# Performance work log

Hardware: AMD Instinct MI355X
Metric: run time of the kernel (lower is better)

## Reference

```python
import jax, jax.numpy as jnp
import numpy as np


def setup_inputs() -> dict:
    key = jax.random.key(0)
    X = jax.random.normal(key, (8, 4096, 64), dtype=jnp.float32)
    return {"X": X}


def reference(X) -> jnp.ndarray:
    # raw_weights: [B, S, S] = X @ X^T
    raw_weights = jnp.einsum("bsd,btd->bst", X, X)
    # softmax over last (key) dim, as in F.softmax(raw_weights, dim=2)
    weights = jax.nn.softmax(raw_weights, axis=2)
    # y: [B, S, D]
    y = jnp.einsum("bst,btd->bsd", weights, X).astype(jnp.float32)
    return y
```

## Files before the change

### kernel.cpp

```cpp
#include <hip/hip_runtime.h>
#include <hip/hip_bf16.h>
#include <stdint.h>


#define BB 8
#define SS 4096
#define DD 64
#define KVB 64
#define LDK 72

typedef __attribute__((ext_vector_type(8))) _Float16 f16x8;
typedef __attribute__((ext_vector_type(8))) __bf16 bf16x8;
typedef __attribute__((ext_vector_type(4))) float f32x4;

__device__ __forceinline__ _Float16 f2h(float f) { return (_Float16)f; }
__device__ __forceinline__ __bf16 f2bf(float f) { return (__bf16)f; }
__device__ __forceinline__ float exp2g(float x) { return __builtin_amdgcn_exp2f(x); }

__device__ __forceinline__ void gload_lds16(const _Float16* g, _Float16* l) {
  __builtin_amdgcn_global_load_lds(
      (const __attribute__((address_space(1))) uint32_t*)g,
      (__attribute__((address_space(3))) uint32_t*)l, 16, 0, 0);
}

__global__ __launch_bounds__(256)
void prepack(const float* __restrict__ X, _Float16* __restrict__ Gh,
             _Float16* __restrict__ Gl, _Float16* __restrict__ Gt) {
  const int b  = blockIdx.x >> 6;
  const int s0 = (blockIdx.x & 63) * 64;
  const int t  = threadIdx.x;
  const int r  = t >> 2;
  const int cq = t & 3;

  __shared__ float Xs[64][68];

  {
    const float* src = X + ((size_t)b * SS + s0 + r) * DD + cq * 16;
    float4 f0 = ((const float4*)src)[0];
    float4 f1 = ((const float4*)src)[1];
    float4 f2 = ((const float4*)src)[2];
    float4 f3 = ((const float4*)src)[3];
    *(float4*)&Xs[r][cq * 16 + 0]  = f0;
    *(float4*)&Xs[r][cq * 16 + 4]  = f1;
    *(float4*)&Xs[r][cq * 16 + 8]  = f2;
    *(float4*)&Xs[r][cq * 16 + 12] = f3;
  }
  __syncthreads();

  const size_t rowbase = ((size_t)b * SS + s0 + r) * DD;
#pragma unroll
  for (int cc = 0; cc < 2; ++cc) {
    const int c = cq * 2 + cc;
    f16x8 h, lo;
#pragma unroll
    for (int j = 0; j < 8; ++j) {
      float v = Xs[r][c * 8 + j];
      _Float16 hv = f2h(v);
      h[j]  = hv;
      lo[j] = f2h(v - (float)hv);
    }
    const int csw = c ^ (r & 7);
    *(f16x8*)(Gh + rowbase + csw * 8) = h;
    *(f16x8*)(Gl + rowbase + csw * 8) = lo;
  }

  const size_t tbase = ((size_t)b * DD + r) * SS + s0;
#pragma unroll
  for (int cc = 0; cc < 2; ++cc) {
    const int c  = cq * 2 + cc;
    const int g  = c >> 2;
    const int qt = c & 3;
    f16x8 h;
#pragma unroll
    for (int j = 0; j < 8; ++j) {
      const int kvl = 32 * g + 16 * (j >> 2) + 4 * qt + (j & 3);
      h[j] = f2h(Xs[kvl][r]);
    }
    const int csw = c ^ (r & 7);
    *(f16x8*)(Gt + tbase + csw * 8) = h;
  }
}

template <int NSPLIT>
__global__ __launch_bounds__(256, 4)
void attn_fwd5(float* __restrict__ Y, const _Float16* __restrict__ Gh,
               const _Float16* __restrict__ Gl, const _Float16* __restrict__ Gt,
               float* __restrict__ Opart, float* __restrict__ ML) {
  const int b    = blockIdx.x & 7;
  const int q0   = ((blockIdx.x >> 3) & 63) * 64;
  const int half = (NSPLIT == 2) ? (blockIdx.x >> 9) : 0;
  const int kvbase = half * (SS / NSPLIT);
  const int NT2    = (SS / NSPLIT) / KVB;

  const int tid  = threadIdx.x;
  const int wid  = tid >> 6;
  const int lane = tid & 63;
  const int lrow = lane & 15;
  const int qt   = lane >> 4;
  const int key  = lane & 7;

  __shared__ __align__(16) _Float16 Kh[2][KVB][DD];
  __shared__ __align__(16) _Float16 Vt[2][DD][KVB];

  const _Float16* GhB = Gh + (size_t)b * SS * DD;
  const _Float16* GlB = Gl + (size_t)b * SS * DD;
  const _Float16* GtB = Gt + (size_t)b * DD * SS;

  const float LOG2E = 1.4426950408889634f;
  f16x8 qh[2], ql[2];
  {
    const int s = q0 + wid * 16 + lrow;
    const _Float16* rh = GhB + (size_t)s * DD;
    const _Float16* rl = GlB + (size_t)s * DD;
#pragma unroll
    for (int kd = 0; kd < 2; ++kd) {
      const int ch = ((kd * 4 + qt) ^ key) * 8;
      f16x8 h  = *(const f16x8*)(rh + ch);
      f16x8 lo = *(const f16x8*)(rl + ch);
#pragma unroll
      for (int j = 0; j < 8; ++j) {
        float q = ((float)h[j] + (float)lo[j]) * LOG2E;
        _Float16 hv = f2h(q);
        qh[kd][j] = hv;
        ql[kd][j] = f2h(q - (float)hv);
      }
    }
  }

  float m = -INFINITY, lsum = 0.f;
  f32x4 accO[4];
#pragma unroll
  for (int dt = 0; dt < 4; ++dt)
#pragma unroll
    for (int r = 0; r < 4; ++r) accO[dt][r] = 0.f;

  const int lr8 = lane >> 3;
  const int co  = (lane & 7) * 8;

  auto stage = [&](int t, int bufi) {
    const int kv0 = kvbase + t * KVB;
#pragma unroll
    for (int i = 0; i < 2; ++i) {
      const int r0 = wid * 16 + i * 8;
      const int gr = kv0 + r0 + lr8;
      gload_lds16(GhB + (size_t)gr * DD + co, &Kh[bufi][r0][0]);
      gload_lds16(GtB + (size_t)(r0 + lr8) * SS + kv0 + co, &Vt[bufi][r0][0]);
    }
  };

  stage(0, 0);
  __syncthreads();

  for (int t = 0; t < NT2; ++t) {
    const int buf = t & 1;
    if (t + 1 < NT2) stage(t + 1, buf ^ 1);

    f32x4 S[4];
#pragma unroll
    for (int s = 0; s < 4; ++s)
#pragma unroll
      for (int r = 0; r < 4; ++r) S[s][r] = 0.f;

    __builtin_amdgcn_s_setprio(1);
#pragma unroll
    for (int kd = 0; kd < 2; ++kd) {
      const int ch = ((kd * 4 + qt) ^ key) * 8;
#pragma unroll
      for (int s = 0; s < 4; ++s) {
        const int row = s * 16 + lrow;
        f16x8 ah = *(const f16x8*)&Kh[buf][row][ch];
        S[s] = __builtin_amdgcn_mfma_f32_16x16x32_f16(ah, qh[kd], S[s], 0, 0, 0);
        S[s] = __builtin_amdgcn_mfma_f32_16x16x32_f16(ah, ql[kd], S[s], 0, 0, 0);
      }
    }
    __builtin_amdgcn_s_setprio(0);

    float v0 = fmaxf(fmaxf(S[0][0], S[0][1]), fmaxf(S[0][2], S[0][3]));
    float v1 = fmaxf(fmaxf(S[1][0], S[1][1]), fmaxf(S[1][2], S[1][3]));
    float v2 = fmaxf(fmaxf(S[2][0], S[2][1]), fmaxf(S[2][2], S[2][3]));
    float v3 = fmaxf(fmaxf(S[3][0], S[3][1]), fmaxf(S[3][2], S[3][3]));
    float vm = fmaxf(fmaxf(v0, v1), fmaxf(v2, v3));
    vm = fmaxf(vm, __shfl_xor(vm, 16));
    vm = fmaxf(vm, __shfl_xor(vm, 32));
    const float mnew = fmaxf(m, vm);
    const float sc   = exp2g(m - mnew);
    m = mnew;

    float rs = 0.f;
#pragma unroll
    for (int s = 0; s < 4; ++s) {
      f32x4 p;
#pragma unroll
      for (int r = 0; r < 4; ++r) p[r] = exp2g(S[s][r] - mnew);
      S[s] = p;
      rs += (p[0] + p[1]) + (p[2] + p[3]);
    }
    rs += __shfl_xor(rs, 16);
    rs += __shfl_xor(rs, 32);
    lsum = lsum * sc + rs;
#pragma unroll
    for (int dt = 0; dt < 4; ++dt)
#pragma unroll
      for (int r = 0; r < 4; ++r) accO[dt][r] *= sc;

    f16x8 pb0, pb1;
#pragma unroll
    for (int j = 0; j < 4; ++j) {
      pb0[j]     = f2h(S[0][j]);
      pb0[j + 4] = f2h(S[1][j]);
      pb1[j]     = f2h(S[2][j]);
      pb1[j + 4] = f2h(S[3][j]);
    }

    __builtin_amdgcn_s_setprio(1);
#pragma unroll
    for (int dt = 0; dt < 4; ++dt) {
      const _Float16* vr = &Vt[buf][dt * 16 + lrow][0];
#pragma unroll
      for (int g = 0; g < 2; ++g) {
        f16x8 av = *(const f16x8*)(vr + ((4 * g + qt) ^ key) * 8);
        accO[dt] = __builtin_amdgcn_mfma_f32_16x16x32_f16(
            av, g ? pb1 : pb0, accO[dt], 0, 0, 0);
      }
    }
    __builtin_amdgcn_s_setprio(0);

    __syncthreads();
  }

  const int srow = q0 + wid * 16 + lrow;
  if (NSPLIT == 1) {
    const float inv = 1.f / lsum;
    float* Yr = Y + ((size_t)b * SS + srow) * DD;
#pragma unroll
    for (int dt = 0; dt < 4; ++dt)
#pragma unroll
      for (int r = 0; r < 4; ++r)
        Yr[dt * 16 + qt * 4 + r] = accO[dt][r] * inv;
  } else {
    float* Or = Opart + (((size_t)half * BB + b) * SS + srow) * DD;
#pragma unroll
    for (int dt = 0; dt < 4; ++dt)
#pragma unroll
      for (int r = 0; r < 4; ++r)
        Or[dt * 16 + qt * 4 + r] = accO[dt][r];
    if (qt == 0) {
      float* mlr = ML + (((size_t)half * BB + b) * SS + srow) * 2;
      mlr[0] = m;
      mlr[1] = lsum;
    }
  }
}

__global__ __launch_bounds__(256)
void combine2(float* __restrict__ Y, const float* __restrict__ Opart,
              const float* __restrict__ ML) {
  const size_t NROW = (size_t)BB * SS;
  const int tid = threadIdx.x;
  const size_t row = (size_t)blockIdx.x * 32 + (tid >> 3);
  const int d0 = (tid & 7) * 8;

  const float m0 = ML[row * 2 + 0];
  const float l0 = ML[row * 2 + 1];
  const float m1 = ML[(NROW + row) * 2 + 0];
  const float l1 = ML[(NROW + row) * 2 + 1];
  const float M  = fmaxf(m0, m1);
  const float w0 = exp2g(m0 - M);
  const float w1 = exp2g(m1 - M);
  const float inv = 1.f / (w0 * l0 + w1 * l1);

  const float* o0 = Opart + row * DD + d0;
  const float* o1 = Opart + (NROW + row) * DD + d0;
  float* y = Y + row * DD + d0;
#pragma unroll
  for (int h = 0; h < 2; ++h) {
    float4 a = ((const float4*)o0)[h];
    float4 c = ((const float4*)o1)[h];
    float4 o;
    o.x = (w0 * a.x + w1 * c.x) * inv;
    o.y = (w0 * a.y + w1 * c.y) * inv;
    o.z = (w0 * a.z + w1 * c.z) * inv;
    o.w = (w0 * a.w + w1 * c.w) * inv;
    ((float4*)y)[h] = o;
  }
}

__global__ __launch_bounds__(256, 2)
void attn_fwd_r2(const float* __restrict__ X, float* __restrict__ Y) {
  const int nqb = SS / 64;
  const int b  = blockIdx.x / nqb;
  const int q0 = (blockIdx.x % nqb) * 64;
  const int tid  = threadIdx.x;
  const int wid  = tid >> 6;
  const int lane = tid & 63;
  const int lrow = lane & 15;
  const int lhi  = lane >> 4;

  __shared__ __align__(16) __bf16 Xh[KVB][LDK];
  __shared__ __align__(16) __bf16 Xl[KVB][LDK];
  __shared__ __align__(16) __bf16 XT[DD][LDK];
  __shared__ __align__(16) __bf16 Pl[4][16][LDK];

  const float* Xb = X + (size_t)b * SS * DD;

  bf16x8 qh[2], ql[2];
  {
    const float* qp = Xb + (size_t)(q0 + wid * 16 + lrow) * DD;
#pragma unroll
    for (int kk = 0; kk < 2; ++kk) {
      const float4* p = reinterpret_cast<const float4*>(qp + kk * 32 + lhi * 8);
      float4 f0 = p[0], f1 = p[1];
      float v[8] = {f0.x, f0.y, f0.z, f0.w, f1.x, f1.y, f1.z, f1.w};
      bf16x8 h, lo;
#pragma unroll
      for (int j = 0; j < 8; ++j) {
        __bf16 hv = f2bf(v[j]);
        h[j]  = hv;
        lo[j] = f2bf(v[j] - (float)hv);
      }
      qh[kk] = h;
      ql[kk] = lo;
    }
  }

  float m[4], lsum[4];
  f32x4 accO[4];
#pragma unroll
  for (int r = 0; r < 4; ++r) { m[r] = -INFINITY; lsum[r] = 0.f; }
#pragma unroll
  for (int c = 0; c < 4; ++c)
#pragma unroll
    for (int r = 0; r < 4; ++r) accO[c][r] = 0.f;

  for (int kv0 = 0; kv0 < SS; kv0 += KVB) {
    __syncthreads();
    {
      const int r  = tid >> 2;
      const int c0 = (tid & 3) * 16;
      const float* src = Xb + (size_t)(kv0 + r) * DD + c0;
#pragma unroll
      for (int half = 0; half < 2; ++half) {
        const float4* p = reinterpret_cast<const float4*>(src + half * 8);
        float4 f0 = p[0], f1 = p[1];
        float v[8] = {f0.x, f0.y, f0.z, f0.w, f1.x, f1.y, f1.z, f1.w};
        bf16x8 h, lo;
#pragma unroll
        for (int j = 0; j < 8; ++j) {
          __bf16 hv = f2bf(v[j]);
          h[j]  = hv;
          lo[j] = f2bf(v[j] - (float)hv);
        }
        *reinterpret_cast<bf16x8*>(&Xh[r][c0 + half * 8]) = h;
        *reinterpret_cast<bf16x8*>(&Xl[r][c0 + half * 8]) = lo;
#pragma unroll
        for (int j = 0; j < 8; ++j) XT[c0 + half * 8 + j][r] = h[j];
      }
    }
    __syncthreads();

    f32x4 Sacc[4];
#pragma unroll
    for (int c = 0; c < 4; ++c)
#pragma unroll
      for (int r = 0; r < 4; ++r) Sacc[c][r] = 0.f;

#pragma unroll
    for (int kk = 0; kk < 2; ++kk) {
#pragma unroll
      for (int c = 0; c < 4; ++c) {
        bf16x8 bh = *reinterpret_cast<bf16x8*>(&Xh[c * 16 + lrow][kk * 32 + lhi * 8]);
        bf16x8 bl = *reinterpret_cast<bf16x8*>(&Xl[c * 16 + lrow][kk * 32 + lhi * 8]);
        Sacc[c] = __builtin_amdgcn_mfma_f32_16x16x32_bf16(qh[kk], bh, Sacc[c], 0, 0, 0);
        Sacc[c] = __builtin_amdgcn_mfma_f32_16x16x32_bf16(qh[kk], bl, Sacc[c], 0, 0, 0);
        Sacc[c] = __builtin_amdgcn_mfma_f32_16x16x32_bf16(ql[kk], bh, Sacc[c], 0, 0, 0);
      }
    }

#pragma unroll
    for (int r = 0; r < 4; ++r) {
      float v = fmaxf(fmaxf(Sacc[0][r], Sacc[1][r]), fmaxf(Sacc[2][r], Sacc[3][r]));
#pragma unroll
      for (int off = 1; off < 16; off <<= 1)
        v = fmaxf(v, __shfl_xor(v, off, 16));
      const float mnew  = fmaxf(m[r], v);
      const float scale = __expf(m[r] - mnew);
      m[r] = mnew;

      float rowsum = 0.f;
#pragma unroll
      for (int c = 0; c < 4; ++c) {
        float p = __expf(Sacc[c][r] - mnew);
        rowsum += p;
        Pl[wid][lhi * 4 + r][c * 16 + lrow] = f2bf(p);
      }
#pragma unroll
      for (int off = 1; off < 16; off <<= 1)
        rowsum += __shfl_xor(rowsum, off, 16);

      lsum[r] = lsum[r] * scale + rowsum;
#pragma unroll
      for (int c = 0; c < 4; ++c) accO[c][r] *= scale;
    }
    __syncthreads();

#pragma unroll
    for (int kk = 0; kk < 2; ++kk) {
      bf16x8 pa = *reinterpret_cast<bf16x8*>(&Pl[wid][lrow][kk * 32 + lhi * 8]);
#pragma unroll
      for (int c = 0; c < 4; ++c) {
        bf16x8 vb = *reinterpret_cast<bf16x8*>(&XT[c * 16 + lrow][kk * 32 + lhi * 8]);
        accO[c] = __builtin_amdgcn_mfma_f32_16x16x32_bf16(pa, vb, accO[c], 0, 0, 0);
      }
    }
  }

  float* Yb = Y + (size_t)b * SS * DD;
  const int rowbase = q0 + wid * 16;
#pragma unroll
  for (int r = 0; r < 4; ++r) {
    const float inv = 1.f / lsum[r];
#pragma unroll
    for (int c = 0; c < 4; ++c) {
      Yb[(size_t)(rowbase + lhi * 4 + r) * DD + c * 16 + lrow] = accO[c][r] * inv;
    }
  }
}

extern "C" void kernel_launch(void* const* d_in, const int* in_sizes, int n_in,
                              void* d_out, int out_size, void* d_ws, size_t ws_size,
                              hipStream_t stream) {
  const float* X = (const float*)d_in[0];
  float* Y = (float*)d_out;

  const size_t elems   = (size_t)BB * SS * DD;
  const size_t packB   = 3 * elems * sizeof(_Float16);
  const size_t opartB  = 2 * elems * sizeof(float);
  const size_t mlB     = 2 * (size_t)BB * SS * 2 * sizeof(float);
  const size_t needSplit = packB + opartB + mlB;

  if (ws_size >= needSplit) {
    _Float16* Gh = (_Float16*)d_ws;
    _Float16* Gl = Gh + elems;
    _Float16* Gt = Gl + elems;
    float* Opart = (float*)((char*)d_ws + packB);
    float* ML    = Opart + 2 * elems;
    prepack<<<dim3(BB * 64), dim3(256), 0, stream>>>(X, Gh, Gl, Gt);
    attn_fwd5<2><<<dim3(2 * BB * (SS / 64)), dim3(256), 0, stream>>>(
        Y, Gh, Gl, Gt, Opart, ML);
    combine2<<<dim3((BB * SS) / 32), dim3(256), 0, stream>>>(Y, Opart, ML);
  } else if (ws_size >= packB) {
    _Float16* Gh = (_Float16*)d_ws;
    _Float16* Gl = Gh + elems;
    _Float16* Gt = Gl + elems;
    prepack<<<dim3(BB * 64), dim3(256), 0, stream>>>(X, Gh, Gl, Gt);
    attn_fwd5<1><<<dim3(BB * (SS / 64)), dim3(256), 0, stream>>>(
        Y, Gh, Gl, Gt, nullptr, nullptr);
  } else {
    attn_fwd_r2<<<dim3(BB * (SS / 64)), dim3(256), 0, stream>>>(X, Y);
  }
}
```

Before: 135.3 us.

## Drop split-Q compensation, add lazy max rescale, store partials in fp16

New measurement: 124.0 us. 8.3% less time.

```diff
diff --git a/kernel.cpp b/kernel.cpp
--- a/kernel.cpp
+++ b/kernel.cpp
@@ -10,6 +10,7 @@
 #define LDK 72
 
 typedef __attribute__((ext_vector_type(8))) _Float16 f16x8;
+typedef __attribute__((ext_vector_type(4))) _Float16 f16x4;
 typedef __attribute__((ext_vector_type(8))) __bf16 bf16x8;
 typedef __attribute__((ext_vector_type(4))) float f32x4;
 
@@ -83,9 +84,9 @@
 
 template <int NSPLIT>
 __global__ __launch_bounds__(256, 4)
-void attn_fwd5(float* __restrict__ Y, const _Float16* __restrict__ Gh,
+void attn_fwd6(float* __restrict__ Y, const _Float16* __restrict__ Gh,
                const _Float16* __restrict__ Gl, const _Float16* __restrict__ Gt,
-               float* __restrict__ Opart, float* __restrict__ ML) {
+               _Float16* __restrict__ Opart, float* __restrict__ ML) {
   const int b    = blockIdx.x & 7;
   const int q0   = ((blockIdx.x >> 3) & 63) * 64;
   const int half = (NSPLIT == 2) ? (blockIdx.x >> 9) : 0;
@@ -107,7 +108,7 @@
   const _Float16* GtB = Gt + (size_t)b * DD * SS;
 
   const float LOG2E = 1.4426950408889634f;
-  f16x8 qh[2], ql[2];
+  f16x8 qf[2];
   {
     const int s = q0 + wid * 16 + lrow;
     const _Float16* rh = GhB + (size_t)s * DD;
@@ -118,12 +119,8 @@
       f16x8 h  = *(const f16x8*)(rh + ch);
       f16x8 lo = *(const f16x8*)(rl + ch);
 #pragma unroll
-      for (int j = 0; j < 8; ++j) {
-        float q = ((float)h[j] + (float)lo[j]) * LOG2E;
-        _Float16 hv = f2h(q);
-        qh[kd][j] = hv;
-        ql[kd][j] = f2h(q - (float)hv);
-      }
+      for (int j = 0; j < 8; ++j)
+        qf[kd][j] = f2h(((float)h[j] + (float)lo[j]) * LOG2E);
     }
   }
 
@@ -151,6 +148,8 @@
   stage(0, 0);
   __syncthreads();
 
+  const float THR = 4.0f;
+
   for (int t = 0; t < NT2; ++t) {
     const int buf = t & 1;
     if (t + 1 < NT2) stage(t + 1, buf ^ 1);
@@ -169,8 +168,7 @@
       for (int s = 0; s < 4; ++s) {
         const int row = s * 16 + lrow;
         f16x8 ah = *(const f16x8*)&Kh[buf][row][ch];
-        S[s] = __builtin_amdgcn_mfma_f32_16x16x32_f16(ah, qh[kd], S[s], 0, 0, 0);
-        S[s] = __builtin_amdgcn_mfma_f32_16x16x32_f16(ah, ql[kd], S[s], 0, 0, 0);
+        S[s] = __builtin_amdgcn_mfma_f32_16x16x32_f16(ah, qf[kd], S[s], 0, 0, 0);
       }
     }
     __builtin_amdgcn_s_setprio(0);
@@ -182,26 +180,30 @@
     float vm = fmaxf(fmaxf(v0, v1), fmaxf(v2, v3));
     vm = fmaxf(vm, __shfl_xor(vm, 16));
     vm = fmaxf(vm, __shfl_xor(vm, 32));
-    const float mnew = fmaxf(m, vm);
-    const float sc   = exp2g(m - mnew);
-    m = mnew;
+
+    if (!__all(vm - m <= THR)) {
+      const float mnew = fmaxf(m, vm);
+      const float sc   = exp2g(m - mnew);
+      m = mnew;
+      lsum *= sc;
+#pragma unroll
+      for (int dt = 0; dt < 4; ++dt)
+#pragma unroll
+        for (int r = 0; r < 4; ++r) accO[dt][r] *= sc;
+    }
 
     float rs = 0.f;
 #pragma unroll
     for (int s = 0; s < 4; ++s) {
       f32x4 p;
 #pragma unroll
-      for (int r = 0; r < 4; ++r) p[r] = exp2g(S[s][r] - mnew);
+      for (int r = 0; r < 4; ++r) p[r] = exp2g(S[s][r] - m);
       S[s] = p;
       rs += (p[0] + p[1]) + (p[2] + p[3]);
     }
     rs += __shfl_xor(rs, 16);
     rs += __shfl_xor(rs, 32);
-    lsum = lsum * sc + rs;
-#pragma unroll
-    for (int dt = 0; dt < 4; ++dt)
-#pragma unroll
-      for (int r = 0; r < 4; ++r) accO[dt][r] *= sc;
+    lsum += rs;
 
     f16x8 pb0, pb1;
 #pragma unroll
@@ -238,12 +240,14 @@
       for (int r = 0; r < 4; ++r)
         Yr[dt * 16 + qt * 4 + r] = accO[dt][r] * inv;
   } else {
-    float* Or = Opart + (((size_t)half * BB + b) * SS + srow) * DD;
-#pragma unroll
-    for (int dt = 0; dt < 4; ++dt)
-#pragma unroll
-      for (int r = 0; r < 4; ++r)
-        Or[dt * 16 + qt * 4 + r] = accO[dt][r];
+    _Float16* Or = Opart + (((size_t)half * BB + b) * SS + srow) * DD;
+#pragma unroll
+    for (int dt = 0; dt < 4; ++dt) {
+      f16x4 o4;
+#pragma unroll
+      for (int r = 0; r < 4; ++r) o4[r] = f2h(accO[dt][r]);
+      *(f16x4*)(Or + dt * 16 + qt * 4) = o4;
+    }
     if (qt == 0) {
       float* mlr = ML + (((size_t)half * BB + b) * SS + srow) * 2;
       mlr[0] = m;
@@ -253,7 +257,7 @@
 }
 
 __global__ __launch_bounds__(256)
-void combine2(float* __restrict__ Y, const float* __restrict__ Opart,
+void combine2(float* __restrict__ Y, const _Float16* __restrict__ Opart,
               const float* __restrict__ ML) {
   const size_t NROW = (size_t)BB * SS;
   const int tid = threadIdx.x;
@@ -269,18 +273,16 @@
   const float w1 = exp2g(m1 - M);
   const float inv = 1.f / (w0 * l0 + w1 * l1);
 
-  const float* o0 = Opart + row * DD + d0;
-  const float* o1 = Opart + (NROW + row) * DD + d0;
+  f16x8 a = *(const f16x8*)(Opart + row * DD + d0);
+  f16x8 c = *(const f16x8*)(Opart + (NROW + row) * DD + d0);
   float* y = Y + row * DD + d0;
 #pragma unroll
   for (int h = 0; h < 2; ++h) {
-    float4 a = ((const float4*)o0)[h];
-    float4 c = ((const float4*)o1)[h];
     float4 o;
-    o.x = (w0 * a.x + w1 * c.x) * inv;
-    o.y = (w0 * a.y + w1 * c.y) * inv;
-    o.z = (w0 * a.z + w1 * c.z) * inv;
-    o.w = (w0 * a.w + w1 * c.w) * inv;
+    o.x = (w0 * (float)a[h * 4 + 0] + w1 * (float)c[h * 4 + 0]) * inv;
+    o.y = (w0 * (float)a[h * 4 + 1] + w1 * (float)c[h * 4 + 1]) * inv;
+    o.z = (w0 * (float)a[h * 4 + 2] + w1 * (float)c[h * 4 + 2]) * inv;
+    o.w = (w0 * (float)a[h * 4 + 3] + w1 * (float)c[h * 4 + 3]) * inv;
     ((float4*)y)[h] = o;
   }
 }
@@ -434,7 +436,7 @@
 
   const size_t elems   = (size_t)BB * SS * DD;
   const size_t packB   = 3 * elems * sizeof(_Float16);
-  const size_t opartB  = 2 * elems * sizeof(float);
+  const size_t opartB  = 2 * elems * sizeof(_Float16);
   const size_t mlB     = 2 * (size_t)BB * SS * 2 * sizeof(float);
   const size_t needSplit = packB + opartB + mlB;
 
@@ -442,10 +444,10 @@
     _Float16* Gh = (_Float16*)d_ws;
     _Float16* Gl = Gh + elems;
     _Float16* Gt = Gl + elems;
-    float* Opart = (float*)((char*)d_ws + packB);
-    float* ML    = Opart + 2 * elems;
+    _Float16* Opart = (_Float16*)((char*)d_ws + packB);
+    float* ML = (float*)((char*)d_ws + packB + opartB);
     prepack<<<dim3(BB * 64), dim3(256), 0, stream>>>(X, Gh, Gl, Gt);
-    attn_fwd5<2><<<dim3(2 * BB * (SS / 64)), dim3(256), 0, stream>>>(
+    attn_fwd6<2><<<dim3(2 * BB * (SS / 64)), dim3(256), 0, stream>>>(
         Y, Gh, Gl, Gt, Opart, ML);
     combine2<<<dim3((BB * SS) / 32), dim3(256), 0, stream>>>(Y, Opart, ML);
   } else if (ws_size >= packB) {
@@ -453,7 +455,7 @@
     _Float16* Gl = Gh + elems;
     _Float16* Gt = Gl + elems;
     prepack<<<dim3(BB * 64), dim3(256), 0, stream>>>(X, Gh, Gl, Gt);
-    attn_fwd5<1><<<dim3(BB * (SS / 64)), dim3(256), 0, stream>>>(
+    attn_fwd6<1><<<dim3(BB * (SS / 64)), dim3(256), 0, stream>>>(
         Y, Gh, Gl, Gt, nullptr, nullptr);
   } else {
     attn_fwd_r2<<<dim3(BB * (SS / 64)), dim3(256), 0, stream>>>(X, Y);
```
